# Kernel optimization log

Measured on AMD Instinct MI355X. Metric: run time of the kernel, lower is better.

Reference implementation:

```python
import jax, jax.numpy as jnp
import numpy as np

B, T, HID = 1, 4096, 1024
H, HKV, D = 16, 4, 64          # query heads, kv heads, head_dim
G = H // HKV                    # gqa groups; repeat '(h g)' -> q head idx = h*G + g
EPS = 1e-6
SCALE = 1.0 / np.sqrt(D)


def setup_inputs() -> dict:
    key = jax.random.key(0)
    ks = jax.random.split(key, 8)
    hidden_states = jax.random.normal(ks[0], (B, T, HID), dtype=jnp.float32)
    # real rotary tables, shape [1, T, D//2]
    inv_freq = 1.0 / (10000.0 ** (jnp.arange(0, D // 2, dtype=jnp.float32) / (D // 2)))
    theta = jnp.arange(T, dtype=jnp.float32)[:, None] * inv_freq[None, :]
    cos = jnp.cos(theta)[None]
    sin = jnp.sin(theta)[None]
    s = 1.0 / np.sqrt(HID)
    Wq = jax.random.normal(ks[1], (HID, H * D), dtype=jnp.float32) * s
    Wk = jax.random.normal(ks[2], (HID, HKV * D), dtype=jnp.float32) * s
    Wv = jax.random.normal(ks[3], (HID, HKV * D), dtype=jnp.float32) * s
    Wo = jax.random.normal(ks[4], (H * D, HID), dtype=jnp.float32) * s
    q_norm_w = jnp.ones((D,), dtype=jnp.float32)
    k_norm_w = jnp.ones((D,), dtype=jnp.float32)
    return dict(hidden_states=hidden_states, cos=cos, sin=sin, Wq=Wq, Wk=Wk,
                Wv=Wv, Wo=Wo, q_norm_w=q_norm_w, k_norm_w=k_norm_w)


def _rmsnorm(x, w):
    xf = x.astype(jnp.float32)
    n = xf * jax.lax.rsqrt(jnp.mean(xf * xf, axis=-1, keepdims=True) + EPS)
    return (n * w).astype(x.dtype)


def _rope(x, cos, sin):
    # x: [b, t, h, d]; cos/sin: [1, t, d//2] -> [1, t, 1, d//2]
    half = x.shape[-1] // 2
    x1, x2 = x[..., :half], x[..., half:]
    c = cos[:, :x.shape[1], None, :]
    s = sin[:, :x.shape[1], None, :]
    return jnp.concatenate([x1 * c - x2 * s, x1 * s + x2 * c], axis=-1)


def reference(hidden_states, cos, sin, Wq, Wk, Wv, Wo, q_norm_w, k_norm_w):
    b, t, _ = hidden_states.shape
    q = (hidden_states @ Wq).reshape(b, t, H, D)
    k = (hidden_states @ Wk).reshape(b, t, HKV, D)
    v = (hidden_states @ Wv).reshape(b, t, HKV, D)
    q = _rmsnorm(q, q_norm_w)
    k = _rmsnorm(k, k_norm_w)
    q = _rope(q, cos, sin)
    k = _rope(k, cos, sin)
    # GQA without materializing repeated K/V: q head idx = kv_head*G + group
    qg = q.reshape(b, t, HKV, G, D)
    scores = jnp.einsum('bqhgd,bkhd->bhgqk', qg, k) * SCALE
    causal = jnp.tril(jnp.ones((t, t), dtype=bool))  # flex block_mask = causal decoder mask
    scores = jnp.where(causal, scores, jnp.finfo(scores.dtype).min)
    p = jax.nn.softmax(scores, axis=-1)
    out = jnp.einsum('bhgqk,bkhd->bqhgd', p, v).reshape(b, t, H * D)
    return out @ Wo
```

## Files before the change

### kernel.cpp

```cpp
#include <hip/hip_runtime.h>
#include <stdint.h>

#define TT 4096
#define HIDD 1024

typedef __attribute__((ext_vector_type(4))) float f32x4;
typedef __attribute__((ext_vector_type(8))) short s16x8;

static constexpr float kEps = 1e-6f;
static constexpr float kCsc = 0.125f * 1.44269504088896f;

static constexpr size_t OFF_HS   = 0;
static constexpr size_t OFF_WQKV = 8388608;
static constexpr size_t OFF_WO   = 11534336;
static constexpr size_t OFF_Q    = 13631488;
static constexpr size_t OFF_K    = 22020096;
static constexpr size_t OFF_O    = 24117248;
static constexpr size_t OFF_VT   = 38797312;

__device__ __forceinline__ unsigned int pk_bf16(float a, float b) {
  union { float f; unsigned int u; } x, y;
  x.f = a; y.f = b;
  unsigned int lo = (x.u + 0x7fffu + ((x.u >> 16) & 1u)) >> 16;
  unsigned int hi = (y.u + 0x7fffu + ((y.u >> 16) & 1u)) >> 16;
  return (lo & 0xffffu) | (hi << 16);
}
__device__ __forceinline__ unsigned int cvtpk(float lo, float hi) {
  unsigned int r;
  asm("v_cvt_pk_bf16_f32 %0, %1, %2" : "=v"(r) : "v"(lo), "v"(hi));
  return r;
}
__device__ __forceinline__ void gload16(const void* g, void* l) {
  __builtin_amdgcn_global_load_lds(
      (const __attribute__((address_space(1))) unsigned int*)g,
      (__attribute__((address_space(3))) unsigned int*)l, 16, 0, 0);
}

__global__ void k_convert_hs(const float* __restrict__ hs, unsigned short* __restrict__ out) {
  int idx = blockIdx.x * 256 + threadIdx.x;
  int t = idx >> 7, kc = idx & 127;
  const float4* src = (const float4*)(hs + (size_t)t * HIDD + kc * 8);
  float4 a = src[0], b = src[1];
  int kcs = (kc & ~7) | ((kc & 7) ^ (t & 7));
  uint4 w;
  w.x = pk_bf16(a.x, a.y); w.y = pk_bf16(a.z, a.w);
  w.z = pk_bf16(b.x, b.y); w.w = pk_bf16(b.z, b.w);
  *(uint4*)(out + (size_t)t * HIDD + kcs * 8) = w;
}

__global__ void k_convert_w_all(const float* __restrict__ Wq, const float* __restrict__ Wk,
                                const float* __restrict__ Wv, const float* __restrict__ Wo,
                                unsigned short* __restrict__ wqkv, unsigned short* __restrict__ wo_t) {
  int b = blockIdx.x, tid = threadIdx.x;
  const float* W; unsigned short* outT; int nshift, idx;
  if (b < 512)      { W = Wq; outT = wqkv;                nshift = 10; idx = b * 256 + tid; }
  else if (b < 640) { W = Wk; outT = wqkv + 1024 * 1024;  nshift = 8;  idx = (b - 512) * 256 + tid; }
  else if (b < 768) { W = Wv; outT = wqkv + 1280 * 1024;  nshift = 8;  idx = (b - 640) * 256 + tid; }
  else              { W = Wo; outT = wo_t;                nshift = 10; idx = (b - 768) * 256 + tid; }
  int ncols = 1 << nshift;
  int kc = idx >> nshift, n = idx & (ncols - 1);
  float v[8];
#pragma unroll
  for (int e = 0; e < 8; ++e) v[e] = W[(size_t)(kc * 8 + e) * ncols + n];
  int kcs = (kc & ~7) | ((kc & 7) ^ (n & 7));
  uint4 w;
  w.x = pk_bf16(v[0], v[1]); w.y = pk_bf16(v[2], v[3]);
  w.z = pk_bf16(v[4], v[5]); w.w = pk_bf16(v[6], v[7]);
  *(uint4*)(outT + (size_t)n * HIDD + kcs * 8) = w;
}

__global__ __launch_bounds__(256) void k_gemm_qkv(const unsigned short* __restrict__ A,
                                                  const unsigned short* __restrict__ Bt,
                                                  const float* __restrict__ cosb,
                                                  const float* __restrict__ sinb,
                                                  const float* __restrict__ qw,
                                                  const float* __restrict__ kw,
                                                  unsigned short* __restrict__ qo,
                                                  unsigned short* __restrict__ ko,
                                                  unsigned short* __restrict__ vt) {
  __shared__ __attribute__((aligned(16))) char smem[49152];
  const int K = HIDD;
  const int tid = threadIdx.x;
  const int m0 = blockIdx.y * 128, slot = blockIdx.x, n0 = slot * 64;
  const int wid = tid >> 6, lane = tid & 63;
  const int g = lane >> 4, qi = lane & 15;
  const int wr = wid >> 1, wc = wid & 1;
  const int srow = lane >> 3, schk = lane & 7;
  f32x4 acc[4][2] = {};
  const int nkt = K >> 6;

  auto STAGE = [&](int b, int k0) {
#pragma unroll
    for (int j = 0; j < 4; ++j) {
      int ra = j * 32 + wid * 8 + srow;
      gload16(A + (size_t)(m0 + ra) * K + k0 + schk * 8,
              smem + b * 16384 + j * 4096 + (wid << 10));
    }
#pragma unroll
    for (int j = 0; j < 2; ++j) {
      int rb = j * 32 + wid * 8 + srow;
      gload16(Bt + (size_t)(n0 + rb) * K + k0 + schk * 8,
              smem + 32768 + b * 8192 + j * 4096 + (wid << 10));
    }
  };

  STAGE(0, 0);
  __syncthreads();
  int cur = 0;
  for (int kt = 0; kt < nkt; ++kt) {
    if (kt + 1 < nkt) STAGE(cur ^ 1, (kt + 1) << 6);
#pragma unroll
    for (int kh = 0; kh < 2; ++kh) {
      s16x8 af[4], bq[2];
#pragma unroll
      for (int i = 0; i < 4; ++i) {
        int rA = wr * 64 + i * 16 + qi;
        af[i] = *(const s16x8*)(smem + cur * 16384 + rA * 128 + ((((kh << 2) | g) ^ (rA & 7)) << 4));
      }
#pragma unroll
      for (int jn = 0; jn < 2; ++jn) {
        int rB = wc * 32 + jn * 16 + qi;
        bq[jn] = *(const s16x8*)(smem + 32768 + cur * 8192 + rB * 128 + ((((kh << 2) | g) ^ (rB & 7)) << 4));
      }
      __builtin_amdgcn_s_setprio(1);
#pragma unroll
      for (int i = 0; i < 4; ++i)
#pragma unroll
        for (int jn = 0; jn < 2; ++jn)
          acc[i][jn] = __builtin_amdgcn_mfma_f32_16x16x32_bf16(af[i], bq[jn], acc[i][jn], 0, 0, 0);
      __builtin_amdgcn_s_setprio(0);
    }
    __syncthreads();
    cur ^= 1;
  }

  float* Cs = (float*)smem;
#pragma unroll
  for (int i = 0; i < 4; ++i)
#pragma unroll
    for (int jn = 0; jn < 2; ++jn) {
      int row = wr * 64 + i * 16 + g * 4;
      int col = wc * 32 + jn * 16 + qi;
#pragma unroll
      for (int r = 0; r < 4; ++r)
        Cs[(row + r) * 66 + col] = acc[i][jn][r];
    }
  __syncthreads();

  if (slot < 20) {
    const int lr = tid >> 1, hf = tid & 1;
    const int t = m0 + lr;
    const float* self_p = Cs + lr * 66 + hf * 32;
    const float* oth_p  = Cs + lr * 66 + (1 - hf) * 32;
    float ss = 0.0f;
#pragma unroll
    for (int e = 0; e < 32; ++e) { float v = self_p[e]; ss += v * v; }
    ss += __shfl_xor(ss, 1);
    const float rms = rsqrtf(ss * (1.0f / 64.0f) + kEps);
    const float* wvec = (slot < 16) ? qw : kw;
    const float outscale = (slot < 16) ? kCsc : 1.0f;
    unsigned int u[16];
#pragma unroll
    for (int ee = 0; ee < 16; ++ee) {
      float o2[2];
#pragma unroll
      for (int p = 0; p < 2; ++p) {
        int e = 2 * ee + p;
        float c = cosb[t * 32 + e];
        float s = sinb[t * 32 + e];
        float self = self_p[e] * rms * wvec[hf * 32 + e];
        float oth  = oth_p[e]  * rms * wvec[(1 - hf) * 32 + e];
        float r = hf ? (oth * s + self * c) : (self * c - oth * s);
        o2[p] = r * outscale;
      }
      u[ee] = cvtpk(o2[0], o2[1]);
    }
    if (slot < 16) {
      unsigned short* base = qo + ((size_t)slot * TT + t) * 64 + hf * 32;
#pragma unroll
      for (int cidx = 0; cidx < 4; ++cidx) {
        uint4 w; w.x = u[cidx * 4]; w.y = u[cidx * 4 + 1]; w.z = u[cidx * 4 + 2]; w.w = u[cidx * 4 + 3];
        *(uint4*)(base + cidx * 8) = w;
      }
    } else {
      const int hv = slot - 16;
      unsigned short* base = ko + ((size_t)hv * TT + t) * 64;
#pragma unroll
      for (int cidx = 0; cidx < 4; ++cidx) {
        int gc = hf * 4 + cidx;
        uint4 w; w.x = u[cidx * 4]; w.y = u[cidx * 4 + 1]; w.z = u[cidx * 4 + 2]; w.w = u[cidx * 4 + 3];
        *(uint4*)(base + (gc ^ (t & 7)) * 8) = w;
      }
    }
  } else {
    const int hv = slot - 20;
#pragma unroll
    for (int tt = 0; tt < 2; ++tt)
#pragma unroll
      for (int jj = 0; jj < 2; ++jj) {
        int idx = jj * 256 + tid;
        int d = idx >> 3, tc = idx & 7;
        uint4 w;
        w.x = cvtpk(Cs[(tt * 64 + tc * 8 + 0) * 66 + d], Cs[(tt * 64 + tc * 8 + 1) * 66 + d]);
        w.y = cvtpk(Cs[(tt * 64 + tc * 8 + 2) * 66 + d], Cs[(tt * 64 + tc * 8 + 3) * 66 + d]);
        w.z = cvtpk(Cs[(tt * 64 + tc * 8 + 4) * 66 + d], Cs[(tt * 64 + tc * 8 + 5) * 66 + d]);
        w.w = cvtpk(Cs[(tt * 64 + tc * 8 + 6) * 66 + d], Cs[(tt * 64 + tc * 8 + 7) * 66 + d]);
        int tcs = tc ^ (d & 7);
        *(uint4*)(vt + ((size_t)hv * 64 + d) * TT + m0 + tt * 64 + tcs * 8) = w;
      }
  }
}

__global__ __launch_bounds__(256) void k_gemm(const unsigned short* __restrict__ A,
                                              const unsigned short* __restrict__ Bt,
                                              float* __restrict__ C, int M, int N, int K) {
  __shared__ __attribute__((aligned(16))) unsigned short As[2][128 * 64];
  __shared__ __attribute__((aligned(16))) unsigned short Bs[2][64 * 64];
  const int tid = threadIdx.x;
  const int m0 = blockIdx.y * 128, n0 = blockIdx.x * 64;
  const int wid = tid >> 6, lane = tid & 63;
  const int g = lane >> 4, qi = lane & 15;
  const int wr = wid >> 1, wc = wid & 1;
  const int srow = lane >> 3, schk = lane & 7;
  f32x4 acc[4][2] = {};
  const int nkt = K >> 6;

  auto STAGE = [&](int b, int k0) {
#pragma unroll
    for (int j = 0; j < 4; ++j) {
      int ra = j * 32 + wid * 8 + srow;
      gload16(A + (size_t)(m0 + ra) * K + k0 + schk * 8,
              (char*)&As[b][0] + j * 4096 + (wid << 10));
    }
#pragma unroll
    for (int j = 0; j < 2; ++j) {
      int rb = j * 32 + wid * 8 + srow;
      gload16(Bt + (size_t)(n0 + rb) * K + k0 + schk * 8,
              (char*)&Bs[b][0] + j * 4096 + (wid << 10));
    }
  };

  STAGE(0, 0);
  __syncthreads();
  int cur = 0;
  for (int kt = 0; kt < nkt; ++kt) {
    if (kt + 1 < nkt) STAGE(cur ^ 1, (kt + 1) << 6);
#pragma unroll
    for (int kh = 0; kh < 2; ++kh) {
      s16x8 af[4], bq[2];
#pragma unroll
      for (int i = 0; i < 4; ++i) {
        int rA = wr * 64 + i * 16 + qi;
        af[i] = *(const s16x8*)((const char*)&As[cur][0] + rA * 128 + ((((kh << 2) | g) ^ (rA & 7)) << 4));
      }
#pragma unroll
      for (int jn = 0; jn < 2; ++jn) {
        int rB = wc * 32 + jn * 16 + qi;
        bq[jn] = *(const s16x8*)((const char*)&Bs[cur][0] + rB * 128 + ((((kh << 2) | g) ^ (rB & 7)) << 4));
      }
      __builtin_amdgcn_s_setprio(1);
#pragma unroll
      for (int i = 0; i < 4; ++i)
#pragma unroll
        for (int jn = 0; jn < 2; ++jn)
          acc[i][jn] = __builtin_amdgcn_mfma_f32_16x16x32_bf16(af[i], bq[jn], acc[i][jn], 0, 0, 0);
      __builtin_amdgcn_s_setprio(0);
    }
    __syncthreads();
    cur ^= 1;
  }
#pragma unroll
  for (int i = 0; i < 4; ++i)
#pragma unroll
    for (int jn = 0; jn < 2; ++jn) {
      int row = m0 + wr * 64 + i * 16 + g * 4;
      int col = n0 + wc * 32 + jn * 16 + qi;
#pragma unroll
      for (int r = 0; r < 4; ++r)
        C[(size_t)(row + r) * N + col] = acc[i][jn][r];
    }
}

__global__ __launch_bounds__(512) void k_attn(const unsigned short* __restrict__ q,
                                              const unsigned short* __restrict__ kk,
                                              const unsigned short* __restrict__ vt,
                                              unsigned short* __restrict__ o) {
  __shared__ __attribute__((aligned(16))) unsigned short Kl[2][64 * 64];
  __shared__ __attribute__((aligned(16))) unsigned short Vl[2][64 * 64];
  __shared__ __attribute__((aligned(16))) unsigned short Pl[8][1536];
  const int tid = threadIdx.x;
  const int bid = blockIdx.x;
  const int work = (bid & 7) * 64 + (bid >> 3);
  const int h = work >> 5;
  const int i0 = work & 31;
  const int hv = h >> 2;
  const int wid = tid >> 6, lane = tid & 63, g = lane >> 4, qi = lane & 15;
  const int qt = (wid < 4) ? i0 : (63 - i0);
  const int smax = 63 - i0;
  char* pb = (char*)&Pl[wid][0];

  auto STAGE = [&](int b, int s) {
    const int kv0 = s * 64;
    const int r = wid * 8 + (lane >> 3), c8 = (lane & 7) * 8;
    gload16(kk + ((size_t)hv * TT + kv0 + r) * 64 + c8, (char*)&Kl[b][0] + (wid << 10));
    gload16(vt + ((size_t)hv * 64 + r) * TT + kv0 + c8, (char*)&Vl[b][0] + (wid << 10));
  };

  const int qg = qt * 64 + (wid & 3) * 16 + qi;
  s16x8 qf[2];
#pragma unroll
  for (int kh = 0; kh < 2; ++kh)
    qf[kh] = *(const s16x8*)(q + ((size_t)h * TT + qg) * 64 + kh * 32 + g * 8);
  f32x4 acc[4] = {};
  float l0 = 0.0f, l1 = 0.0f;

  STAGE(0, 0);
  __syncthreads();
  int cur = 0;
  for (int s = 0; s <= smax; ++s) {
    if (s < smax) STAGE(cur ^ 1, s + 1);
    if (s <= qt) {
      const int kv0 = s * 64;
      f32x4 sacc[4] = {};
#pragma unroll
      for (int kh = 0; kh < 2; ++kh) {
        s16x8 kf[4];
#pragma unroll
        for (int cf = 0; cf < 4; ++cf) {
          int row = cf * 16 + qi;
          kf[cf] = *(const s16x8*)((const char*)&Kl[cur][0] + row * 128 + ((((kh << 2) | g) ^ (row & 7)) << 4));
        }
        __builtin_amdgcn_s_setprio(1);
#pragma unroll
        for (int cf = 0; cf < 4; ++cf)
          sacc[cf] = __builtin_amdgcn_mfma_f32_16x16x32_bf16(kf[cf], qf[kh], sacc[cf], 0, 0, 0);
        __builtin_amdgcn_s_setprio(0);
      }
      float pv[16];
      if (s == qt) {
#pragma unroll
        for (int cf = 0; cf < 4; ++cf)
#pragma unroll
          for (int r = 0; r < 4; ++r) {
            float v = sacc[cf][r];
            if ((kv0 + cf * 16 + g * 4 + r) > qg) v = -1e30f;
            pv[cf * 4 + r] = v;
          }
      } else {
#pragma unroll
        for (int cf = 0; cf < 4; ++cf)
#pragma unroll
          for (int r = 0; r < 4; ++r) pv[cf * 4 + r] = sacc[cf][r];
      }
#pragma unroll
      for (int i = 0; i < 8; ++i) {
        float e0 = exp2f(pv[2 * i]), e1 = exp2f(pv[2 * i + 1]);
        pv[2 * i] = e0; pv[2 * i + 1] = e1;
        l0 += e0; l1 += e1;
      }
#pragma unroll
      for (int cf = 0; cf < 4; ++cf) {
        int chunk = cf * 2 + (g >> 1);
        int base = qi * 128 + ((chunk ^ (qi & 7)) << 4) + ((g & 1) << 3);
        uint2 pw;
        pw.x = cvtpk(pv[cf * 4 + 0], pv[cf * 4 + 1]);
        pw.y = cvtpk(pv[cf * 4 + 2], pv[cf * 4 + 3]);
        *(uint2*)(pb + base) = pw;
      }
#pragma unroll
      for (int kh = 0; kh < 2; ++kh) {
        s16x8 pf = *(const s16x8*)(pb + qi * 128 + ((((kh << 2) | g) ^ (qi & 7)) << 4));
        s16x8 vf[4];
#pragma unroll
        for (int cf = 0; cf < 4; ++cf) {
          int row = cf * 16 + qi;
          vf[cf] = *(const s16x8*)((const char*)&Vl[cur][0] + row * 128 + ((((kh << 2) | g) ^ (row & 7)) << 4));
        }
        __builtin_amdgcn_s_setprio(1);
#pragma unroll
        for (int cf = 0; cf < 4; ++cf)
          acc[cf] = __builtin_amdgcn_mfma_f32_16x16x32_bf16(vf[cf], pf, acc[cf], 0, 0, 0);
        __builtin_amdgcn_s_setprio(0);
      }
    }
    __syncthreads();
    cur ^= 1;
  }
  float l_run = l0 + l1;
  l_run += __shfl_xor(l_run, 16);
  l_run += __shfl_xor(l_run, 32);
  float inv = 1.0f / l_run;
#pragma unroll
  for (int cf = 0; cf < 4; ++cf) {
    int col = h * 64 + cf * 16 + g * 4;
    int chunk = col >> 3;
    int chs = (chunk & ~7) | ((chunk & 7) ^ (qg & 7));
    char* ob = (char*)o + (size_t)qg * 2048 + (chs << 4) + ((g & 1) << 3);
    *(unsigned int*)ob = cvtpk(acc[cf][0] * inv, acc[cf][1] * inv);
    *(unsigned int*)(ob + 4) = cvtpk(acc[cf][2] * inv, acc[cf][3] * inv);
  }
}

extern "C" void kernel_launch(void* const* d_in, const int* in_sizes, int n_in,
                              void* d_out, int out_size, void* d_ws, size_t ws_size,
                              hipStream_t stream) {
  const float* hs   = (const float*)d_in[0];
  const float* cosb = (const float*)d_in[1];
  const float* sinb = (const float*)d_in[2];
  const float* Wq   = (const float*)d_in[3];
  const float* Wk   = (const float*)d_in[4];
  const float* Wv   = (const float*)d_in[5];
  const float* Wo   = (const float*)d_in[6];
  const float* qw   = (const float*)d_in[7];
  const float* kw   = (const float*)d_in[8];
  char* ws = (char*)d_ws;
  unsigned short* hs_swz = (unsigned short*)(ws + OFF_HS);
  unsigned short* wqkv   = (unsigned short*)(ws + OFF_WQKV);
  unsigned short* wo_t   = (unsigned short*)(ws + OFF_WO);
  unsigned short* qbf    = (unsigned short*)(ws + OFF_Q);
  unsigned short* kbf    = (unsigned short*)(ws + OFF_K);
  unsigned short* vtb    = (unsigned short*)(ws + OFF_VT);
  unsigned short* obf    = (unsigned short*)(ws + OFF_O);

  k_convert_hs<<<2048, 256, 0, stream>>>(hs, hs_swz);
  k_convert_w_all<<<1280, 256, 0, stream>>>(Wq, Wk, Wv, Wo, wqkv, wo_t);
  k_gemm_qkv<<<dim3(24, 32), 256, 0, stream>>>(hs_swz, wqkv, cosb, sinb, qw, kw, qbf, kbf, vtb);
  k_attn<<<512, 512, 0, stream>>>(qbf, kbf, vtb, obf);
  k_gemm<<<dim3(16, 32), 256, 0, stream>>>(obf, wo_t, (float*)d_out, 4096, 1024, 1024);
}
```

Measured before the change: 131.1 us.

## Split causal attention KV range across blocks with atomic fp32 accumulation and normalize pass

```diff
diff --git a/kernel.cpp b/kernel.cpp
--- a/kernel.cpp
+++ b/kernel.cpp
@@ -5,6 +5,7 @@
 #define HIDD 1024
 
 typedef __attribute__((ext_vector_type(4))) float f32x4;
+typedef __attribute__((ext_vector_type(16))) float f32x16;
 typedef __attribute__((ext_vector_type(8))) short s16x8;
 
 static constexpr float kEps = 1e-6f;
@@ -12,11 +13,13 @@
 
 static constexpr size_t OFF_HS   = 0;
 static constexpr size_t OFF_WQKV = 8388608;
-static constexpr size_t OFF_WO   = 11534336;
-static constexpr size_t OFF_Q    = 13631488;
-static constexpr size_t OFF_K    = 22020096;
-static constexpr size_t OFF_O    = 24117248;
-static constexpr size_t OFF_VT   = 38797312;
+static constexpr size_t OFF_OBUF = 0;
+static constexpr size_t OFF_LBUF = 16777216;
+static constexpr size_t OFF_WO   = 17039360;
+static constexpr size_t OFF_Q    = 19136512;
+static constexpr size_t OFF_K    = 27525120;
+static constexpr size_t OFF_VT   = 29622272;
+static constexpr size_t OFF_O    = 31719424;
 
 __device__ __forceinline__ unsigned int pk_bf16(float a, float b) {
   union { float f; unsigned int u; } x, y;
@@ -281,124 +284,141 @@
     }
 }
 
-__global__ __launch_bounds__(512) void k_attn(const unsigned short* __restrict__ q,
-                                              const unsigned short* __restrict__ kk,
-                                              const unsigned short* __restrict__ vt,
-                                              unsigned short* __restrict__ o) {
-  __shared__ __attribute__((aligned(16))) unsigned short Kl[2][64 * 64];
-  __shared__ __attribute__((aligned(16))) unsigned short Vl[2][64 * 64];
-  __shared__ __attribute__((aligned(16))) unsigned short Pl[8][1536];
+__global__ __launch_bounds__(256, 2) void k_attn(const unsigned short* __restrict__ q,
+                                                 const unsigned short* __restrict__ kk,
+                                                 const unsigned short* __restrict__ vt,
+                                                 float* __restrict__ obuf,
+                                                 float* __restrict__ lbuf) {
+  __shared__ __attribute__((aligned(16))) char smem[57344];
   const int tid = threadIdx.x;
+  const int wid = tid >> 6, lane = tid & 63;
+  const int ln31 = lane & 31, hi = lane >> 5;
   const int bid = blockIdx.x;
-  const int work = (bid & 7) * 64 + (bid >> 3);
-  const int h = work >> 5;
-  const int i0 = work & 31;
-  const int hv = h >> 2;
-  const int wid = tid >> 6, lane = tid & 63, g = lane >> 4, qi = lane & 15;
-  const int qt = (wid < 4) ? i0 : (63 - i0);
-  const int smax = 63 - i0;
-  char* pb = (char*)&Pl[wid][0];
-
-  auto STAGE = [&](int b, int s) {
-    const int kv0 = s * 64;
-    const int r = wid * 8 + (lane >> 3), c8 = (lane & 7) * 8;
-    gload16(kk + ((size_t)hv * TT + kv0 + r) * 64 + c8, (char*)&Kl[b][0] + (wid << 10));
-    gload16(vt + ((size_t)hv * 64 + r) * TT + kv0 + c8, (char*)&Vl[b][0] + (wid << 10));
+  const int xcd = bid & 7;
+  const int rdec = bid >> 3;
+  const int head = xcd * 2 + (rdec >> 5);
+  const int rr = rdec & 31;
+  const int j = rr >> 1, half = rr & 1;
+  const int hv = head >> 2;
+
+  auto STAGE = [&](int b, int kvt) {
+    const int kv0 = kvt * 64;
+#pragma unroll
+    for (int p = 0; p < 2; ++p) {
+      int c = tid + p * 256;
+      int row = c >> 3, ch = c & 7;
+      gload16(kk + ((size_t)hv * TT + kv0 + row) * 64 + ch * 8,
+              smem + b * 8192 + c * 16);
+      gload16(vt + ((size_t)hv * 64 + row) * TT + kv0 + ch * 8,
+              smem + 16384 + b * 8192 + c * 16);
+    }
   };
 
-  const int qg = qt * 64 + (wid & 3) * 16 + qi;
-  s16x8 qf[2];
-#pragma unroll
-  for (int kh = 0; kh < 2; ++kh)
-    qf[kh] = *(const s16x8*)(q + ((size_t)h * TT + qg) * 64 + kh * 32 + g * 8);
-  f32x4 acc[4] = {};
-  float l0 = 0.0f, l1 = 0.0f;
-
-  STAGE(0, 0);
-  __syncthreads();
-  int cur = 0;
-  for (int s = 0; s <= smax; ++s) {
-    if (s < smax) STAGE(cur ^ 1, s + 1);
-    if (s <= qt) {
-      const int kv0 = s * 64;
-      f32x4 sacc[4] = {};
-#pragma unroll
-      for (int kh = 0; kh < 2; ++kh) {
-        s16x8 kf[4];
-#pragma unroll
-        for (int cf = 0; cf < 4; ++cf) {
-          int row = cf * 16 + qi;
-          kf[cf] = *(const s16x8*)((const char*)&Kl[cur][0] + row * 128 + ((((kh << 2) | g) ^ (row & 7)) << 4));
+#pragma unroll
+  for (int phase = 0; phase < 2; ++phase) {
+    const int band = phase ? j : (31 - j);
+    const int len  = phase ? (j + 1) : (32 - j);
+    const int kvlo = half * len;
+    const int qb = band * 128 + wid * 32;
+    const int diagT = qb >> 6;
+    const int qg = qb + ln31;
+
+    s16x8 qf[4];
+#pragma unroll
+    for (int ks = 0; ks < 4; ++ks)
+      qf[ks] = *(const s16x8*)(q + ((size_t)head * TT + qb + ln31) * 64 + ks * 16 + hi * 8);
+
+    f32x16 oacc[2] = {};
+    float lp0 = 0.0f, lp1 = 0.0f;
+
+    STAGE(0, kvlo);
+    __syncthreads();
+    int cur = 0;
+    for (int ss = 0; ss < len; ++ss) {
+      if (ss + 1 < len) STAGE(cur ^ 1, kvlo + ss + 1);
+      const int kvt = kvlo + ss;
+      if (kvt <= diagT) {
+        const int kv0 = kvt * 64;
+        const char* Kb = smem + cur * 8192;
+        const char* Vb = smem + 16384 + cur * 8192;
+        f32x16 sacc[2] = {};
+#pragma unroll
+        for (int T = 0; T < 2; ++T) {
+#pragma unroll
+          for (int ks = 0; ks < 4; ++ks) {
+            int row = T * 32 + ln31;
+            s16x8 kf = *(const s16x8*)(Kb + row * 128 + (((2 * ks + hi) ^ (row & 7)) << 4));
+            sacc[T] = __builtin_amdgcn_mfma_f32_32x32x16_bf16(kf, qf[ks], sacc[T], 0, 0, 0);
+          }
         }
-        __builtin_amdgcn_s_setprio(1);
-#pragma unroll
-        for (int cf = 0; cf < 4; ++cf)
-          sacc[cf] = __builtin_amdgcn_mfma_f32_16x16x32_bf16(kf[cf], qf[kh], sacc[cf], 0, 0, 0);
-        __builtin_amdgcn_s_setprio(0);
-      }
-      float pv[16];
-      if (s == qt) {
-#pragma unroll
-        for (int cf = 0; cf < 4; ++cf)
-#pragma unroll
-          for (int r = 0; r < 4; ++r) {
-            float v = sacc[cf][r];
-            if ((kv0 + cf * 16 + g * 4 + r) > qg) v = -1e30f;
-            pv[cf * 4 + r] = v;
+        float pv[32];
+        const bool diag = (kvt == diagT);
+#pragma unroll
+        for (int T = 0; T < 2; ++T)
+#pragma unroll
+          for (int r = 0; r < 16; ++r) {
+            float v = sacc[T][r];
+            if (diag) {
+              int kvg = kv0 + T * 32 + (r & 3) + 8 * (r >> 2) + 4 * hi;
+              if (kvg > qg) v = -1e30f;
+            }
+            float e = exp2f(v);
+            pv[T * 16 + r] = e;
+            if (r & 1) lp1 += e; else lp0 += e;
           }
-      } else {
-#pragma unroll
-        for (int cf = 0; cf < 4; ++cf)
-#pragma unroll
-          for (int r = 0; r < 4; ++r) pv[cf * 4 + r] = sacc[cf][r];
-      }
-#pragma unroll
-      for (int i = 0; i < 8; ++i) {
-        float e0 = exp2f(pv[2 * i]), e1 = exp2f(pv[2 * i + 1]);
-        pv[2 * i] = e0; pv[2 * i + 1] = e1;
-        l0 += e0; l1 += e1;
-      }
-#pragma unroll
-      for (int cf = 0; cf < 4; ++cf) {
-        int chunk = cf * 2 + (g >> 1);
-        int base = qi * 128 + ((chunk ^ (qi & 7)) << 4) + ((g & 1) << 3);
-        uint2 pw;
-        pw.x = cvtpk(pv[cf * 4 + 0], pv[cf * 4 + 1]);
-        pw.y = cvtpk(pv[cf * 4 + 2], pv[cf * 4 + 3]);
-        *(uint2*)(pb + base) = pw;
-      }
-#pragma unroll
-      for (int kh = 0; kh < 2; ++kh) {
-        s16x8 pf = *(const s16x8*)(pb + qi * 128 + ((((kh << 2) | g) ^ (qi & 7)) << 4));
-        s16x8 vf[4];
-#pragma unroll
-        for (int cf = 0; cf < 4; ++cf) {
-          int row = cf * 16 + qi;
-          vf[cf] = *(const s16x8*)((const char*)&Vl[cur][0] + row * 128 + ((((kh << 2) | g) ^ (row & 7)) << 4));
+        s16x8 pa[4];
+#pragma unroll
+        for (int ks = 0; ks < 4; ++ks) {
+          const float* pg = pv + ks * 8;
+          unsigned w0 = cvtpk(pg[0], pg[1]);
+          unsigned w1 = cvtpk(pg[2], pg[3]);
+          unsigned w2 = cvtpk(pg[4], pg[5]);
+          unsigned w3 = cvtpk(pg[6], pg[7]);
+          asm("v_permlane32_swap_b32 %0, %1" : "+v"(w0), "+v"(w2));
+          asm("v_permlane32_swap_b32 %0, %1" : "+v"(w1), "+v"(w3));
+          union { uint4 u4; s16x8 v8; } cc;
+          cc.u4.x = w0; cc.u4.y = w1; cc.u4.z = w2; cc.u4.w = w3;
+          pa[ks] = cc.v8;
         }
-        __builtin_amdgcn_s_setprio(1);
-#pragma unroll
-        for (int cf = 0; cf < 4; ++cf)
-          acc[cf] = __builtin_amdgcn_mfma_f32_16x16x32_bf16(vf[cf], pf, acc[cf], 0, 0, 0);
-        __builtin_amdgcn_s_setprio(0);
-      }
-    }
-    __syncthreads();
-    cur ^= 1;
+#pragma unroll
+        for (int D = 0; D < 2; ++D) {
+#pragma unroll
+          for (int ks = 0; ks < 4; ++ks) {
+            int row = D * 32 + ln31;
+            s16x8 vf = *(const s16x8*)(Vb + row * 128 + (((2 * ks + hi) ^ (row & 7)) << 4));
+            oacc[D] = __builtin_amdgcn_mfma_f32_32x32x16_bf16(pa[ks], vf, oacc[D], 0, 0, 0);
+          }
+        }
+      }
+      __syncthreads();
+      cur ^= 1;
+    }
+    float lfull = lp0 + lp1;
+    lfull += __shfl_xor(lfull, 32);
+    if (hi == 0)
+      unsafeAtomicAdd(lbuf + (size_t)head * TT + qb + ln31, lfull);
+#pragma unroll
+    for (int r = 0; r < 16; ++r) {
+      int qoff = (r & 3) + 8 * (r >> 2) + 4 * hi;
+#pragma unroll
+      for (int D = 0; D < 2; ++D)
+        unsafeAtomicAdd(obuf + (size_t)(qb + qoff) * 1024 + head * 64 + D * 32 + ln31, oacc[D][r]);
+    }
   }
-  float l_run = l0 + l1;
-  l_run += __shfl_xor(l_run, 16);
-  l_run += __shfl_xor(l_run, 32);
-  float inv = 1.0f / l_run;
-#pragma unroll
-  for (int cf = 0; cf < 4; ++cf) {
-    int col = h * 64 + cf * 16 + g * 4;
-    int chunk = col >> 3;
-    int chs = (chunk & ~7) | ((chunk & 7) ^ (qg & 7));
-    char* ob = (char*)o + (size_t)qg * 2048 + (chs << 4) + ((g & 1) << 3);
-    *(unsigned int*)ob = cvtpk(acc[cf][0] * inv, acc[cf][1] * inv);
-    *(unsigned int*)(ob + 4) = cvtpk(acc[cf][2] * inv, acc[cf][3] * inv);
-  }
+}
+
+__global__ void k_norm(const float* __restrict__ obuf, const float* __restrict__ lbuf,
+                       unsigned short* __restrict__ obf) {
+  int idx = blockIdx.x * 256 + threadIdx.x;
+  int t = idx >> 7, kc = idx & 127;
+  const float4* src = (const float4*)(obuf + (size_t)t * 1024 + kc * 8);
+  float inv = 1.0f / lbuf[(size_t)(kc >> 3) * TT + t];
+  float4 a = src[0], b = src[1];
+  uint4 w;
+  w.x = cvtpk(a.x * inv, a.y * inv); w.y = cvtpk(a.z * inv, a.w * inv);
+  w.z = cvtpk(b.x * inv, b.y * inv); w.w = cvtpk(b.z * inv, b.w * inv);
+  int kcs = (kc & ~7) | ((kc & 7) ^ (t & 7));
+  *(uint4*)(obf + (size_t)t * 1024 + kcs * 8) = w;
 }
 
 extern "C" void kernel_launch(void* const* d_in, const int* in_sizes, int n_in,
@@ -416,6 +436,8 @@
   char* ws = (char*)d_ws;
   unsigned short* hs_swz = (unsigned short*)(ws + OFF_HS);
   unsigned short* wqkv   = (unsigned short*)(ws + OFF_WQKV);
+  float*          obuf   = (float*)(ws + OFF_OBUF);
+  float*          lbuf   = (float*)(ws + OFF_LBUF);
   unsigned short* wo_t   = (unsigned short*)(ws + OFF_WO);
   unsigned short* qbf    = (unsigned short*)(ws + OFF_Q);
   unsigned short* kbf    = (unsigned short*)(ws + OFF_K);
@@ -425,6 +447,9 @@
   k_convert_hs<<<2048, 256, 0, stream>>>(hs, hs_swz);
   k_convert_w_all<<<1280, 256, 0, stream>>>(Wq, Wk, Wv, Wo, wqkv, wo_t);
   k_gemm_qkv<<<dim3(24, 32), 256, 0, stream>>>(hs_swz, wqkv, cosb, sinb, qw, kw, qbf, kbf, vtb);
-  k_attn<<<512, 512, 0, stream>>>(qbf, kbf, vtb, obf);
+  hipMemsetAsync(obuf, 0, (size_t)4096 * 1024 * 4, stream);
+  hipMemsetAsync(lbuf, 0, (size_t)16 * 4096 * 4, stream);
+  k_attn<<<512, 256, 0, stream>>>(qbf, kbf, vtb, obuf, lbuf);
+  k_norm<<<2048, 256, 0, stream>>>(obuf, lbuf, obf);
   k_gemm<<<dim3(16, 32), 256, 0, stream>>>(obf, wo_t, (float*)d_out, 4096, 1024, 1024);
 }
```

Result: slower. 148.0 us (+12.9%).

## Split attention KV range across two blocks with atomic accumulation and normalize pass

Applied to the files above, without the earlier changes.

```diff
diff --git a/kernel.cpp b/kernel.cpp
--- a/kernel.cpp
+++ b/kernel.cpp
@@ -12,11 +12,13 @@
 
 static constexpr size_t OFF_HS   = 0;
 static constexpr size_t OFF_WQKV = 8388608;
-static constexpr size_t OFF_WO   = 11534336;
-static constexpr size_t OFF_Q    = 13631488;
-static constexpr size_t OFF_K    = 22020096;
-static constexpr size_t OFF_O    = 24117248;
-static constexpr size_t OFF_VT   = 38797312;
+static constexpr size_t OFF_OBUF = 0;
+static constexpr size_t OFF_LBUF = 16777216;
+static constexpr size_t OFF_WO   = 17039360;
+static constexpr size_t OFF_Q    = 19136512;
+static constexpr size_t OFF_K    = 27525120;
+static constexpr size_t OFF_VT   = 29622272;
+static constexpr size_t OFF_O    = 31719424;
 
 __device__ __forceinline__ unsigned int pk_bf16(float a, float b) {
   union { float f; unsigned int u; } x, y;
@@ -281,46 +283,53 @@
     }
 }
 
-__global__ __launch_bounds__(512) void k_attn(const unsigned short* __restrict__ q,
-                                              const unsigned short* __restrict__ kk,
-                                              const unsigned short* __restrict__ vt,
-                                              unsigned short* __restrict__ o) {
-  __shared__ __attribute__((aligned(16))) unsigned short Kl[2][64 * 64];
-  __shared__ __attribute__((aligned(16))) unsigned short Vl[2][64 * 64];
-  __shared__ __attribute__((aligned(16))) unsigned short Pl[8][1536];
+__global__ __launch_bounds__(512, 8) void k_attn(const unsigned short* __restrict__ q,
+                                                 const unsigned short* __restrict__ kk,
+                                                 const unsigned short* __restrict__ vt,
+                                                 float* __restrict__ obuf,
+                                                 float* __restrict__ lbuf) {
+  __shared__ __attribute__((aligned(16))) char smem[40960];
   const int tid = threadIdx.x;
+  const int wid = tid >> 6, lane = tid & 63, g = lane >> 4, qi = lane & 15;
   const int bid = blockIdx.x;
-  const int work = (bid & 7) * 64 + (bid >> 3);
-  const int h = work >> 5;
-  const int i0 = work & 31;
-  const int hv = h >> 2;
-  const int wid = tid >> 6, lane = tid & 63, g = lane >> 4, qi = lane & 15;
-  const int qt = (wid < 4) ? i0 : (63 - i0);
-  const int smax = 63 - i0;
-  char* pb = (char*)&Pl[wid][0];
-
-  auto STAGE = [&](int b, int s) {
-    const int kv0 = s * 64;
-    const int r = wid * 8 + (lane >> 3), c8 = (lane & 7) * 8;
-    gload16(kk + ((size_t)hv * TT + kv0 + r) * 64 + c8, (char*)&Kl[b][0] + (wid << 10));
-    gload16(vt + ((size_t)hv * 64 + r) * TT + kv0 + c8, (char*)&Vl[b][0] + (wid << 10));
+  const int xcd = bid & 7;
+  const int rem = bid >> 3;
+  const int b_ord = rem >> 2, sub = rem & 3;
+  const int head = xcd * 2 + (sub >> 1);
+  const int half = sub & 1;
+  const int band = 31 - b_ord;
+  const int len = band + 1;
+  const int kvlo = half * len;
+  const int hv = head >> 2;
+  char* pb = smem + 32768 + (wid << 10);
+
+  auto STAGE = [&](int b, int kvt) {
+    const int row = tid >> 3, ch = tid & 7;
+    gload16(kk + ((size_t)hv * TT + kvt * 64 + row) * 64 + ch * 8,
+            smem + b * 8192 + tid * 16);
+    gload16(vt + ((size_t)hv * 64 + row) * TT + kvt * 64 + ch * 8,
+            smem + 16384 + b * 8192 + tid * 16);
   };
 
-  const int qg = qt * 64 + (wid & 3) * 16 + qi;
+  const int qg = band * 128 + wid * 16 + qi;
+  const int diagT = 2 * band + (wid >> 2);
   s16x8 qf[2];
 #pragma unroll
   for (int kh = 0; kh < 2; ++kh)
-    qf[kh] = *(const s16x8*)(q + ((size_t)h * TT + qg) * 64 + kh * 32 + g * 8);
+    qf[kh] = *(const s16x8*)(q + ((size_t)head * TT + qg) * 64 + kh * 32 + g * 8);
   f32x4 acc[4] = {};
   float l0 = 0.0f, l1 = 0.0f;
 
-  STAGE(0, 0);
+  STAGE(0, kvlo);
   __syncthreads();
   int cur = 0;
-  for (int s = 0; s <= smax; ++s) {
-    if (s < smax) STAGE(cur ^ 1, s + 1);
-    if (s <= qt) {
-      const int kv0 = s * 64;
+  for (int ss = 0; ss < len; ++ss) {
+    if (ss + 1 < len) STAGE(cur ^ 1, kvlo + ss + 1);
+    const int kvt = kvlo + ss;
+    if (kvt <= diagT) {
+      const int kv0 = kvt * 64;
+      const char* Kb = smem + cur * 8192;
+      const char* Vb = smem + 16384 + cur * 8192;
       f32x4 sacc[4] = {};
 #pragma unroll
       for (int kh = 0; kh < 2; ++kh) {
@@ -328,7 +337,7 @@
 #pragma unroll
         for (int cf = 0; cf < 4; ++cf) {
           int row = cf * 16 + qi;
-          kf[cf] = *(const s16x8*)((const char*)&Kl[cur][0] + row * 128 + ((((kh << 2) | g) ^ (row & 7)) << 4));
+          kf[cf] = *(const s16x8*)(Kb + row * 128 + ((((kh << 2) | g) ^ (row & 7)) << 4));
         }
         __builtin_amdgcn_s_setprio(1);
 #pragma unroll
@@ -337,7 +346,7 @@
         __builtin_amdgcn_s_setprio(0);
       }
       float pv[16];
-      if (s == qt) {
+      if (kvt == diagT) {
 #pragma unroll
         for (int cf = 0; cf < 4; ++cf)
 #pragma unroll
@@ -359,22 +368,21 @@
         l0 += e0; l1 += e1;
       }
 #pragma unroll
-      for (int cf = 0; cf < 4; ++cf) {
-        int chunk = cf * 2 + (g >> 1);
-        int base = qi * 128 + ((chunk ^ (qi & 7)) << 4) + ((g & 1) << 3);
-        uint2 pw;
-        pw.x = cvtpk(pv[cf * 4 + 0], pv[cf * 4 + 1]);
-        pw.y = cvtpk(pv[cf * 4 + 2], pv[cf * 4 + 3]);
-        *(uint2*)(pb + base) = pw;
-      }
-#pragma unroll
       for (int kh = 0; kh < 2; ++kh) {
-        s16x8 pf = *(const s16x8*)(pb + qi * 128 + ((((kh << 2) | g) ^ (qi & 7)) << 4));
+#pragma unroll
+        for (int cl = 0; cl < 2; ++cl) {
+          int cf = 2 * kh + cl;
+          uint2 pw;
+          pw.x = cvtpk(pv[cf * 4 + 0], pv[cf * 4 + 1]);
+          pw.y = cvtpk(pv[cf * 4 + 2], pv[cf * 4 + 3]);
+          *(uint2*)(pb + qi * 64 + cl * 32 + g * 8) = pw;
+        }
+        s16x8 pf = *(const s16x8*)(pb + qi * 64 + g * 16);
         s16x8 vf[4];
 #pragma unroll
         for (int cf = 0; cf < 4; ++cf) {
           int row = cf * 16 + qi;
-          vf[cf] = *(const s16x8*)((const char*)&Vl[cur][0] + row * 128 + ((((kh << 2) | g) ^ (row & 7)) << 4));
+          vf[cf] = *(const s16x8*)(Vb + row * 128 + ((((kh << 2) | g) ^ (row & 7)) << 4));
         }
         __builtin_amdgcn_s_setprio(1);
 #pragma unroll
@@ -389,16 +397,27 @@
   float l_run = l0 + l1;
   l_run += __shfl_xor(l_run, 16);
   l_run += __shfl_xor(l_run, 32);
-  float inv = 1.0f / l_run;
-#pragma unroll
-  for (int cf = 0; cf < 4; ++cf) {
-    int col = h * 64 + cf * 16 + g * 4;
-    int chunk = col >> 3;
-    int chs = (chunk & ~7) | ((chunk & 7) ^ (qg & 7));
-    char* ob = (char*)o + (size_t)qg * 2048 + (chs << 4) + ((g & 1) << 3);
-    *(unsigned int*)ob = cvtpk(acc[cf][0] * inv, acc[cf][1] * inv);
-    *(unsigned int*)(ob + 4) = cvtpk(acc[cf][2] * inv, acc[cf][3] * inv);
-  }
+  if (lane < 16)
+    unsafeAtomicAdd(lbuf + (size_t)head * TT + band * 128 + wid * 16 + qi, l_run);
+#pragma unroll
+  for (int cf = 0; cf < 4; ++cf)
+#pragma unroll
+    for (int r = 0; r < 4; ++r)
+      unsafeAtomicAdd(obuf + (size_t)qg * 1024 + head * 64 + cf * 16 + g * 4 + r, acc[cf][r]);
+}
+
+__global__ void k_norm(const float* __restrict__ obuf, const float* __restrict__ lbuf,
+                       unsigned short* __restrict__ obf) {
+  int idx = blockIdx.x * 256 + threadIdx.x;
+  int t = idx >> 7, kc = idx & 127;
+  const float4* src = (const float4*)(obuf + (size_t)t * 1024 + kc * 8);
+  float inv = 1.0f / lbuf[(size_t)(kc >> 3) * TT + t];
+  float4 a = src[0], b = src[1];
+  uint4 w;
+  w.x = cvtpk(a.x * inv, a.y * inv); w.y = cvtpk(a.z * inv, a.w * inv);
+  w.z = cvtpk(b.x * inv, b.y * inv); w.w = cvtpk(b.z * inv, b.w * inv);
+  int kcs = (kc & ~7) | ((kc & 7) ^ (t & 7));
+  *(uint4*)(obf + (size_t)t * 1024 + kcs * 8) = w;
 }
 
 extern "C" void kernel_launch(void* const* d_in, const int* in_sizes, int n_in,
@@ -416,6 +435,8 @@
   char* ws = (char*)d_ws;
   unsigned short* hs_swz = (unsigned short*)(ws + OFF_HS);
   unsigned short* wqkv   = (unsigned short*)(ws + OFF_WQKV);
+  float*          obuf   = (float*)(ws + OFF_OBUF);
+  float*          lbuf   = (float*)(ws + OFF_LBUF);
   unsigned short* wo_t   = (unsigned short*)(ws + OFF_WO);
   unsigned short* qbf    = (unsigned short*)(ws + OFF_Q);
   unsigned short* kbf    = (unsigned short*)(ws + OFF_K);
@@ -425,6 +446,9 @@
   k_convert_hs<<<2048, 256, 0, stream>>>(hs, hs_swz);
   k_convert_w_all<<<1280, 256, 0, stream>>>(Wq, Wk, Wv, Wo, wqkv, wo_t);
   k_gemm_qkv<<<dim3(24, 32), 256, 0, stream>>>(hs_swz, wqkv, cosb, sinb, qw, kw, qbf, kbf, vtb);
-  k_attn<<<512, 512, 0, stream>>>(qbf, kbf, vtb, obf);
+  hipMemsetAsync(obuf, 0, (size_t)4096 * 1024 * 4, stream);
+  hipMemsetAsync(lbuf, 0, (size_t)16 * 4096 * 4, stream);
+  k_attn<<<1024, 512, 0, stream>>>(qbf, kbf, vtb, obuf, lbuf);
+  k_norm<<<2048, 256, 0, stream>>>(obuf, lbuf, obf);
   k_gemm<<<dim3(16, 32), 256, 0, stream>>>(obf, wo_t, (float*)d_out, 4096, 1024, 1024);
 }
```

New measurement: 287.8 us. 120% more time.

## Split attention into one-query-tile blocks, scheduled longest-first, instead of paired tiles

Applied to the files above, without the earlier changes.

```diff
diff --git a/kernel.cpp b/kernel.cpp
--- a/kernel.cpp
+++ b/kernel.cpp
@@ -281,107 +281,108 @@
     }
 }
 
-__global__ __launch_bounds__(512) void k_attn(const unsigned short* __restrict__ q,
+__global__ __launch_bounds__(256) void k_attn(const unsigned short* __restrict__ q,
                                               const unsigned short* __restrict__ kk,
                                               const unsigned short* __restrict__ vt,
                                               unsigned short* __restrict__ o) {
   __shared__ __attribute__((aligned(16))) unsigned short Kl[2][64 * 64];
   __shared__ __attribute__((aligned(16))) unsigned short Vl[2][64 * 64];
-  __shared__ __attribute__((aligned(16))) unsigned short Pl[8][1536];
+  __shared__ __attribute__((aligned(16))) unsigned short Pl[4][1024];
   const int tid = threadIdx.x;
+  const int wid = tid >> 6, lane = tid & 63, g = lane >> 4, qi = lane & 15;
   const int bid = blockIdx.x;
-  const int work = (bid & 7) * 64 + (bid >> 3);
-  const int h = work >> 5;
-  const int i0 = work & 31;
-  const int hv = h >> 2;
-  const int wid = tid >> 6, lane = tid & 63, g = lane >> 4, qi = lane & 15;
-  const int qt = (wid < 4) ? i0 : (63 - i0);
-  const int smax = 63 - i0;
+  const int xcd = bid & 7;
+  const int rem = bid >> 3;
+  const int head = xcd * 2 + (rem & 1);
+  const int qt = 63 - (rem >> 1);
+  const int hv = head >> 2;
   char* pb = (char*)&Pl[wid][0];
 
   auto STAGE = [&](int b, int s) {
     const int kv0 = s * 64;
-    const int r = wid * 8 + (lane >> 3), c8 = (lane & 7) * 8;
-    gload16(kk + ((size_t)hv * TT + kv0 + r) * 64 + c8, (char*)&Kl[b][0] + (wid << 10));
-    gload16(vt + ((size_t)hv * 64 + r) * TT + kv0 + c8, (char*)&Vl[b][0] + (wid << 10));
+#pragma unroll
+    for (int p = 0; p < 2; ++p) {
+      int c = tid + p * 256;
+      int r = c >> 3, ch8 = (c & 7) * 8;
+      gload16(kk + ((size_t)hv * TT + kv0 + r) * 64 + ch8, (char*)&Kl[b][0] + c * 16);
+      gload16(vt + ((size_t)hv * 64 + r) * TT + kv0 + ch8, (char*)&Vl[b][0] + c * 16);
+    }
   };
 
-  const int qg = qt * 64 + (wid & 3) * 16 + qi;
+  const int qg = qt * 64 + wid * 16 + qi;
   s16x8 qf[2];
 #pragma unroll
   for (int kh = 0; kh < 2; ++kh)
-    qf[kh] = *(const s16x8*)(q + ((size_t)h * TT + qg) * 64 + kh * 32 + g * 8);
+    qf[kh] = *(const s16x8*)(q + ((size_t)head * TT + qg) * 64 + kh * 32 + g * 8);
   f32x4 acc[4] = {};
   float l0 = 0.0f, l1 = 0.0f;
 
   STAGE(0, 0);
   __syncthreads();
   int cur = 0;
-  for (int s = 0; s <= smax; ++s) {
-    if (s < smax) STAGE(cur ^ 1, s + 1);
-    if (s <= qt) {
-      const int kv0 = s * 64;
-      f32x4 sacc[4] = {};
-#pragma unroll
-      for (int kh = 0; kh < 2; ++kh) {
-        s16x8 kf[4];
-#pragma unroll
-        for (int cf = 0; cf < 4; ++cf) {
-          int row = cf * 16 + qi;
-          kf[cf] = *(const s16x8*)((const char*)&Kl[cur][0] + row * 128 + ((((kh << 2) | g) ^ (row & 7)) << 4));
+  for (int s = 0; s <= qt; ++s) {
+    if (s < qt) STAGE(cur ^ 1, s + 1);
+    const int kv0 = s * 64;
+    f32x4 sacc[4] = {};
+#pragma unroll
+    for (int kh = 0; kh < 2; ++kh) {
+      s16x8 kf[4];
+#pragma unroll
+      for (int cf = 0; cf < 4; ++cf) {
+        int row = cf * 16 + qi;
+        kf[cf] = *(const s16x8*)((const char*)&Kl[cur][0] + row * 128 + ((((kh << 2) | g) ^ (row & 7)) << 4));
+      }
+      __builtin_amdgcn_s_setprio(1);
+#pragma unroll
+      for (int cf = 0; cf < 4; ++cf)
+        sacc[cf] = __builtin_amdgcn_mfma_f32_16x16x32_bf16(kf[cf], qf[kh], sacc[cf], 0, 0, 0);
+      __builtin_amdgcn_s_setprio(0);
+    }
+    float pv[16];
+    if (s == qt) {
+#pragma unroll
+      for (int cf = 0; cf < 4; ++cf)
+#pragma unroll
+        for (int r = 0; r < 4; ++r) {
+          float v = sacc[cf][r];
+          if ((kv0 + cf * 16 + g * 4 + r) > qg) v = -1e30f;
+          pv[cf * 4 + r] = v;
         }
-        __builtin_amdgcn_s_setprio(1);
-#pragma unroll
-        for (int cf = 0; cf < 4; ++cf)
-          sacc[cf] = __builtin_amdgcn_mfma_f32_16x16x32_bf16(kf[cf], qf[kh], sacc[cf], 0, 0, 0);
-        __builtin_amdgcn_s_setprio(0);
-      }
-      float pv[16];
-      if (s == qt) {
-#pragma unroll
-        for (int cf = 0; cf < 4; ++cf)
-#pragma unroll
-          for (int r = 0; r < 4; ++r) {
-            float v = sacc[cf][r];
-            if ((kv0 + cf * 16 + g * 4 + r) > qg) v = -1e30f;
-            pv[cf * 4 + r] = v;
-          }
-      } else {
-#pragma unroll
-        for (int cf = 0; cf < 4; ++cf)
-#pragma unroll
-          for (int r = 0; r < 4; ++r) pv[cf * 4 + r] = sacc[cf][r];
-      }
-#pragma unroll
-      for (int i = 0; i < 8; ++i) {
-        float e0 = exp2f(pv[2 * i]), e1 = exp2f(pv[2 * i + 1]);
-        pv[2 * i] = e0; pv[2 * i + 1] = e1;
-        l0 += e0; l1 += e1;
-      }
+    } else {
+#pragma unroll
+      for (int cf = 0; cf < 4; ++cf)
+#pragma unroll
+        for (int r = 0; r < 4; ++r) pv[cf * 4 + r] = sacc[cf][r];
+    }
+#pragma unroll
+    for (int i = 0; i < 8; ++i) {
+      float e0 = exp2f(pv[2 * i]), e1 = exp2f(pv[2 * i + 1]);
+      pv[2 * i] = e0; pv[2 * i + 1] = e1;
+      l0 += e0; l1 += e1;
+    }
+#pragma unroll
+    for (int cf = 0; cf < 4; ++cf) {
+      int chunk = cf * 2 + (g >> 1);
+      int base = qi * 128 + ((chunk ^ (qi & 7)) << 4) + ((g & 1) << 3);
+      uint2 pw;
+      pw.x = cvtpk(pv[cf * 4 + 0], pv[cf * 4 + 1]);
+      pw.y = cvtpk(pv[cf * 4 + 2], pv[cf * 4 + 3]);
+      *(uint2*)(pb + base) = pw;
+    }
+#pragma unroll
+    for (int kh = 0; kh < 2; ++kh) {
+      s16x8 pf = *(const s16x8*)(pb + qi * 128 + ((((kh << 2) | g) ^ (qi & 7)) << 4));
+      s16x8 vf[4];
 #pragma unroll
       for (int cf = 0; cf < 4; ++cf) {
-        int chunk = cf * 2 + (g >> 1);
-        int base = qi * 128 + ((chunk ^ (qi & 7)) << 4) + ((g & 1) << 3);
-        uint2 pw;
-        pw.x = cvtpk(pv[cf * 4 + 0], pv[cf * 4 + 1]);
-        pw.y = cvtpk(pv[cf * 4 + 2], pv[cf * 4 + 3]);
-        *(uint2*)(pb + base) = pw;
-      }
-#pragma unroll
-      for (int kh = 0; kh < 2; ++kh) {
-        s16x8 pf = *(const s16x8*)(pb + qi * 128 + ((((kh << 2) | g) ^ (qi & 7)) << 4));
-        s16x8 vf[4];
-#pragma unroll
-        for (int cf = 0; cf < 4; ++cf) {
-          int row = cf * 16 + qi;
-          vf[cf] = *(const s16x8*)((const char*)&Vl[cur][0] + row * 128 + ((((kh << 2) | g) ^ (row & 7)) << 4));
-        }
-        __builtin_amdgcn_s_setprio(1);
-#pragma unroll
-        for (int cf = 0; cf < 4; ++cf)
-          acc[cf] = __builtin_amdgcn_mfma_f32_16x16x32_bf16(vf[cf], pf, acc[cf], 0, 0, 0);
-        __builtin_amdgcn_s_setprio(0);
-      }
+        int row = cf * 16 + qi;
+        vf[cf] = *(const s16x8*)((const char*)&Vl[cur][0] + row * 128 + ((((kh << 2) | g) ^ (row & 7)) << 4));
+      }
+      __builtin_amdgcn_s_setprio(1);
+#pragma unroll
+      for (int cf = 0; cf < 4; ++cf)
+        acc[cf] = __builtin_amdgcn_mfma_f32_16x16x32_bf16(vf[cf], pf, acc[cf], 0, 0, 0);
+      __builtin_amdgcn_s_setprio(0);
     }
     __syncthreads();
     cur ^= 1;
@@ -392,7 +393,7 @@
   float inv = 1.0f / l_run;
 #pragma unroll
   for (int cf = 0; cf < 4; ++cf) {
-    int col = h * 64 + cf * 16 + g * 4;
+    int col = head * 64 + cf * 16 + g * 4;
     int chunk = col >> 3;
     int chs = (chunk & ~7) | ((chunk & 7) ^ (qg & 7));
     char* ob = (char*)o + (size_t)qg * 2048 + (chs << 4) + ((g & 1) << 3);
@@ -425,6 +426,6 @@
   k_convert_hs<<<2048, 256, 0, stream>>>(hs, hs_swz);
   k_convert_w_all<<<1280, 256, 0, stream>>>(Wq, Wk, Wv, Wo, wqkv, wo_t);
   k_gemm_qkv<<<dim3(24, 32), 256, 0, stream>>>(hs_swz, wqkv, cosb, sinb, qw, kw, qbf, kbf, vtb);
-  k_attn<<<512, 512, 0, stream>>>(qbf, kbf, vtb, obf);
+  k_attn<<<1024, 256, 0, stream>>>(qbf, kbf, vtb, obf);
   k_gemm<<<dim3(16, 32), 256, 0, stream>>>(obf, wo_t, (float*)d_out, 4096, 1024, 1024);
 }
```

After: 133.6 us. No clear change (+1.9%).
